# Kernel optimization log

Measured on AMD Instinct MI355X. Metric: run time of the kernel, lower is better.

The kernel has to match this reference:

```python
import jax, jax.numpy as jnp
import numpy as np

B, N, DM, H, C, DC = 4, 1024, 512, 8, 3, 16  # batch, nodes, node_dim, heads, manifold components, per-component dim
DK = DM // H


def setup_inputs() -> dict:
    key = jax.random.key(0)
    ks = jax.random.split(key, 8)

    def lin_w(k):
        return jax.random.normal(k, (DM, DM), jnp.float32) / np.sqrt(DM).astype(np.float32)

    return {
        "h": jax.random.normal(ks[0], (B, N, DM), jnp.float32),
        "x": jax.random.normal(ks[1], (B, N, C * DC), jnp.float32),
        "Wq": lin_w(ks[2]), "bq": jnp.zeros((DM,), jnp.float32),
        "Wk": lin_w(ks[3]), "bk": jnp.zeros((DM,), jnp.float32),
        "Wv": lin_w(ks[4]), "bv": jnp.zeros((DM,), jnp.float32),
        "Wo": lin_w(ks[5]), "bo": jnp.zeros((DM,), jnp.float32),
        "alpha": jnp.ones((H, C), jnp.float32),
        "log_sigma": jnp.zeros((H, C), jnp.float32),
    }


def reference(h, x, Wq, bq, Wk, bk, Wv, bv, Wo, bo, alpha, log_sigma):
    b, n, dm = h.shape
    hh, cc = alpha.shape
    dk = dm // hh
    scale = 1.0 / np.sqrt(dk).astype(np.float32)

    def to_heads(t, W, bias):
        return (t @ W.T + bias).reshape(b, n, hh, dk).transpose(0, 2, 1, 3)  # (B,H,N,dk)

    Q = to_heads(h, Wq, bq)
    K = to_heads(h, Wk, bk)
    V = to_heads(h, Wv, bv)

    attn = jnp.einsum('bhid,bhjd->bhij', Q, K) * scale  # (B,H,N,N)

    # Geodesic kernel: per-component Euclidean distances on the product manifold.
    xs = x.reshape(b, n, cc, -1)                      # (B,N,C,dc)
    sq = jnp.sum(xs * xs, axis=-1)                    # (B,N,C)
    inner = jnp.einsum('bicd,bjcd->bijc', xs, xs)     # (B,N,N,C)
    d_sq = jnp.maximum(sq[:, :, None, :] + sq[:, None, :, :] - 2.0 * inner, 0.0)  # (B,N,N,C)

    sigma = jnp.clip(jnp.exp(log_sigma), 1e-4)        # (H,C)
    # exp(-d_c^2 / (2 sigma_{h,c}^2)) -> (B,H,N,N,C), then weight by alpha and sum over c
    e = jnp.exp(-d_sq[:, None] / (2.0 * (sigma ** 2)[None, :, None, None, :])).astype(attn.dtype)
    attn = attn + jnp.einsum('hc,bhijc->bhij', alpha, e)

    p = jax.nn.softmax(attn, axis=-1)
    out = jnp.einsum('bhij,bhjd->bhid', p, V)         # (B,H,N,dk)
    out = out.transpose(0, 2, 1, 3).reshape(b, n, dm)
    return out @ Wo.T + bo
```

## Files before the change

kernel.cpp:

```cpp
#include <hip/hip_runtime.h>

typedef __bf16 bf16;
typedef __attribute__((ext_vector_type(8))) __bf16 bf16x8;
typedef __attribute__((ext_vector_type(4))) float f32x4;

#define LOG2E 1.44269504088896f
#define SCALE 0.125f

__device__ inline f32x4 mfma16(bf16x8 a, bf16x8 b, f32x4 c) {
    return __builtin_amdgcn_mfma_f32_16x16x32_bf16(a, b, c, 0, 0, 0);
}

__global__ __launch_bounds__(256) void prep_kernel(
        const float* __restrict__ h, const float* __restrict__ x,
        const float* __restrict__ Wq, const float* __restrict__ Wk,
        const float* __restrict__ Wv, const float* __restrict__ Wo,
        const float* __restrict__ bq, const float* __restrict__ bk,
        const float* __restrict__ bv,
        bf16* __restrict__ hb, bf16* __restrict__ wpack, bf16* __restrict__ wob,
        float* __restrict__ bqkv, bf16* __restrict__ xb, float* __restrict__ sqx) {
    int stride = gridDim.x * blockDim.x;
    int tid = blockIdx.x * blockDim.x + threadIdx.x;
    for (int i = tid; i < 4096 * 512; i += stride) hb[i] = (bf16)h[i];
    for (int i = tid; i < 3 * 512 * 512; i += stride) {
        float v = (i < 262144) ? Wq[i] : (i < 524288 ? Wk[i - 262144] : Wv[i - 524288]);
        wpack[i] = (bf16)v;
    }
    for (int i = tid; i < 512 * 512; i += stride) wob[i] = (bf16)Wo[i];
    for (int i = tid; i < 1536; i += stride)
        bqkv[i] = (i < 512) ? bq[i] : (i < 1024 ? bk[i - 512] : bv[i - 1024]);
    for (int i = tid; i < 4096 * 48; i += stride) xb[i] = (bf16)x[i];
    for (int i = tid; i < 4096 * 3; i += stride) {
        int row = i / 3, c = i - row * 3;
        float s = 0.0f;
        for (int k = 0; k < 16; k++) {
            float v = (float)(bf16)x[row * 48 + c * 16 + k];
            s += v * v;
        }
        sqx[i] = s;
    }
}

__global__ __launch_bounds__(256) void gemm_qkv_kernel(
        const bf16* __restrict__ A, const bf16* __restrict__ Bm,
        const float* __restrict__ bias,
        bf16* __restrict__ Qb, bf16* __restrict__ Kb, bf16* __restrict__ Vb) {
    __shared__ bf16 Al[64][72];
    __shared__ bf16 Bl[64][72];
    int t = threadIdx.x;
    int w = t >> 6, lane = t & 63, g = lane >> 4, lo = lane & 15;
    int rowbase = blockIdx.x * 64, colbase = blockIdx.y * 64;
    int wr = (w >> 1) * 32, wc = (w & 1) * 32;
    f32x4 acc[2][2] = {};
    int sr = t >> 2, sc = (t & 3) * 16;
    for (int kb = 0; kb < 512; kb += 64) {
        *(bf16x8*)&Al[sr][sc]     = *(const bf16x8*)&A[(rowbase + sr) * 512 + kb + sc];
        *(bf16x8*)&Al[sr][sc + 8] = *(const bf16x8*)&A[(rowbase + sr) * 512 + kb + sc + 8];
        *(bf16x8*)&Bl[sr][sc]     = *(const bf16x8*)&Bm[(colbase + sr) * 512 + kb + sc];
        *(bf16x8*)&Bl[sr][sc + 8] = *(const bf16x8*)&Bm[(colbase + sr) * 512 + kb + sc + 8];
        __syncthreads();
        for (int kk = 0; kk < 64; kk += 32) {
            bf16x8 af[2], bfr[2];
            af[0]  = *(const bf16x8*)&Al[wr + lo][kk + 8 * g];
            af[1]  = *(const bf16x8*)&Al[wr + 16 + lo][kk + 8 * g];
            bfr[0] = *(const bf16x8*)&Bl[wc + lo][kk + 8 * g];
            bfr[1] = *(const bf16x8*)&Bl[wc + 16 + lo][kk + 8 * g];
            for (int ri = 0; ri < 2; ri++)
                for (int ci = 0; ci < 2; ci++)
                    acc[ri][ci] = mfma16(af[ri], bfr[ci], acc[ri][ci]);
        }
        __syncthreads();
    }
    for (int ri = 0; ri < 2; ri++)
        for (int ci = 0; ci < 2; ci++) {
            int mcol = colbase + wc + 16 * ci + lo;
            float bv = bias[mcol];
            int proj = mcol >> 9, hm = mcol & 511, head = hm >> 6, d = hm & 63;
            bf16* dst = (proj == 0) ? Qb : (proj == 1 ? Kb : Vb);
            for (int r = 0; r < 4; r++) {
                int n = rowbase + wr + 16 * ri + 4 * g + r;
                int bidx = n >> 10, i = n & 1023;
                dst[((bidx * 8 + head) * 1024 + i) * 64 + d] = (bf16)(acc[ri][ci][r] + bv);
            }
        }
}

__global__ __launch_bounds__(256) void attn_kernel(
        const bf16* __restrict__ Qb, const bf16* __restrict__ Kb,
        const bf16* __restrict__ Vb, const bf16* __restrict__ xb,
        const float* __restrict__ sqx, const float* __restrict__ alpha,
        const float* __restrict__ log_sigma, bf16* __restrict__ attnout) {
    __shared__ bf16 Klds[64][72];
    __shared__ bf16 Xlds[64][56];
    __shared__ bf16 VTlds[64][72];
    __shared__ float sqj[3][64];
    __shared__ bf16 Plds[4][16][72];

    int t = threadIdx.x;
    int w = t >> 6, lane = t & 63, g = lane >> 4, lo = lane & 15;
    int b = blockIdx.z, hh = blockIdx.y;
    int i0 = blockIdx.x * 64 + w * 16;

    float alf[3], coef[3];
    for (int c = 0; c < 3; c++) {
        alf[c] = alpha[hh * 3 + c];
        float sg = expf(log_sigma[hh * 3 + c]);
        sg = fmaxf(sg, 1e-4f);
        coef[c] = -LOG2E / (2.0f * sg * sg);
    }

    const bf16* Qbase = Qb + ((size_t)(b * 8 + hh) * 1024 + i0) * 64;
    bf16x8 qa[2];
    qa[0] = *(const bf16x8*)&Qbase[lo * 64 + 8 * g];
    qa[1] = *(const bf16x8*)&Qbase[lo * 64 + 32 + 8 * g];

    bf16x8 xqa[3];
    const bf16* Xibase = xb + ((size_t)(b << 10) + i0) * 48;
    for (int c = 0; c < 3; c++) {
        bf16x8 v = {};
        if (g < 2) v = *(const bf16x8*)&Xibase[lo * 48 + c * 16 + 8 * g];
        xqa[c] = v;
    }

    float sqi[3][4];
    const float* sqibase = sqx + ((size_t)(b << 10) + i0) * 3;
    for (int r = 0; r < 4; r++)
        for (int c = 0; c < 3; c++) sqi[c][r] = sqibase[(4 * g + r) * 3 + c];

    float m_r[4], l_r[4];
    f32x4 o[4];
    for (int r = 0; r < 4; r++) { m_r[r] = -1e30f; l_r[r] = 0.0f; }
    for (int td = 0; td < 4; td++) o[td] = (f32x4){0.f, 0.f, 0.f, 0.f};

    int sr = t >> 2, sc = (t & 3) * 16;
    for (int j0 = 0; j0 < 1024; j0 += 64) {
        __syncthreads();
        const bf16* Kbase = Kb + ((size_t)(b * 8 + hh) * 1024 + j0) * 64;
        *(bf16x8*)&Klds[sr][sc]     = *(const bf16x8*)&Kbase[sr * 64 + sc];
        *(bf16x8*)&Klds[sr][sc + 8] = *(const bf16x8*)&Kbase[sr * 64 + sc + 8];
        const bf16* Vbase = Vb + ((size_t)(b * 8 + hh) * 1024 + j0) * 64;
        bf16x8 v0 = *(const bf16x8*)&Vbase[sr * 64 + sc];
        bf16x8 v1 = *(const bf16x8*)&Vbase[sr * 64 + sc + 8];
        for (int q = 0; q < 8; q++) VTlds[sc + q][sr] = v0[q];
        for (int q = 0; q < 8; q++) VTlds[sc + 8 + q][sr] = v1[q];
        for (int idx = t; idx < 384; idx += 256) {
            int xr = idx / 6, xc = (idx - xr * 6) * 8;
            *(bf16x8*)&Xlds[xr][xc] = *(const bf16x8*)&xb[((size_t)(b << 10) + j0 + xr) * 48 + xc];
        }
        if (t < 192) {
            int jl = t / 3, c = t - jl * 3;
            sqj[c][jl] = sqx[((size_t)(b << 10) + j0 + jl) * 3 + c];
        }
        __syncthreads();

        f32x4 s[4];
        for (int tt = 0; tt < 4; tt++) {
            f32x4 acc = {};
            bf16x8 kb0 = *(const bf16x8*)&Klds[16 * tt + lo][8 * g];
            bf16x8 kb1 = *(const bf16x8*)&Klds[16 * tt + lo][32 + 8 * g];
            acc = mfma16(qa[0], kb0, acc);
            acc = mfma16(qa[1], kb1, acc);
            f32x4 ic[3];
            for (int c = 0; c < 3; c++) {
                bf16x8 xbf = {};
                if (g < 2) xbf = *(const bf16x8*)&Xlds[16 * tt + lo][c * 16 + 8 * g];
                f32x4 z = {};
                ic[c] = mfma16(xqa[c], xbf, z);
            }
            for (int r = 0; r < 4; r++) {
                float sv = acc[r] * SCALE;
                for (int c = 0; c < 3; c++) {
                    float d = sqi[c][r] + sqj[c][16 * tt + lo] - 2.0f * ic[c][r];
                    d = fmaxf(d, 0.0f);
                    sv += alf[c] * exp2f(coef[c] * d);
                }
                acc[r] = sv;
            }
            s[tt] = acc;
        }

        float pm[4], sf[4], rs[4];
        for (int r = 0; r < 4; r++)
            pm[r] = fmaxf(fmaxf(s[0][r], s[1][r]), fmaxf(s[2][r], s[3][r]));
        for (int msk = 1; msk < 16; msk <<= 1)
            for (int r = 0; r < 4; r++) pm[r] = fmaxf(pm[r], __shfl_xor(pm[r], msk));
        for (int r = 0; r < 4; r++) {
            float mn = fmaxf(m_r[r], pm[r]);
            sf[r] = exp2f((m_r[r] - mn) * LOG2E);
            m_r[r] = mn;
            rs[r] = 0.0f;
        }
        for (int tt = 0; tt < 4; tt++)
            for (int r = 0; r < 4; r++) {
                float p = exp2f((s[tt][r] - m_r[r]) * LOG2E);
                s[tt][r] = p;
                rs[r] += p;
            }
        for (int msk = 1; msk < 16; msk <<= 1)
            for (int r = 0; r < 4; r++) rs[r] += __shfl_xor(rs[r], msk);
        for (int r = 0; r < 4; r++) l_r[r] = l_r[r] * sf[r] + rs[r];

        for (int tt = 0; tt < 4; tt++)
            for (int r = 0; r < 4; r++)
                Plds[w][4 * g + r][16 * tt + lo] = (bf16)s[tt][r];

        for (int td = 0; td < 4; td++)
            for (int r = 0; r < 4; r++) o[td][r] *= sf[r];

        bf16x8 pa0 = *(const bf16x8*)&Plds[w][lo][8 * g];
        bf16x8 pa1 = *(const bf16x8*)&Plds[w][lo][32 + 8 * g];
        for (int td = 0; td < 4; td++) {
            bf16x8 vb0 = *(const bf16x8*)&VTlds[16 * td + lo][8 * g];
            bf16x8 vb1 = *(const bf16x8*)&VTlds[16 * td + lo][32 + 8 * g];
            o[td] = mfma16(pa0, vb0, o[td]);
            o[td] = mfma16(pa1, vb1, o[td]);
        }
    }

    for (int td = 0; td < 4; td++)
        for (int r = 0; r < 4; r++) {
            float val = o[td][r] / l_r[r];
            int i = i0 + 4 * g + r;
            attnout[((size_t)(b << 10) + i) * 512 + hh * 64 + 16 * td + lo] = (bf16)val;
        }
}

__global__ __launch_bounds__(256) void gemm_out_kernel(
        const bf16* __restrict__ A, const bf16* __restrict__ Bm,
        const float* __restrict__ bias, float* __restrict__ out) {
    __shared__ bf16 Al[64][72];
    __shared__ bf16 Bl[64][72];
    int t = threadIdx.x;
    int w = t >> 6, lane = t & 63, g = lane >> 4, lo = lane & 15;
    int rowbase = blockIdx.x * 64, colbase = blockIdx.y * 64;
    int wr = (w >> 1) * 32, wc = (w & 1) * 32;
    f32x4 acc[2][2] = {};
    int sr = t >> 2, sc = (t & 3) * 16;
    for (int kb = 0; kb < 512; kb += 64) {
        *(bf16x8*)&Al[sr][sc]     = *(const bf16x8*)&A[(rowbase + sr) * 512 + kb + sc];
        *(bf16x8*)&Al[sr][sc + 8] = *(const bf16x8*)&A[(rowbase + sr) * 512 + kb + sc + 8];
        *(bf16x8*)&Bl[sr][sc]     = *(const bf16x8*)&Bm[(colbase + sr) * 512 + kb + sc];
        *(bf16x8*)&Bl[sr][sc + 8] = *(const bf16x8*)&Bm[(colbase + sr) * 512 + kb + sc + 8];
        __syncthreads();
        for (int kk = 0; kk < 64; kk += 32) {
            bf16x8 af[2], bfr[2];
            af[0]  = *(const bf16x8*)&Al[wr + lo][kk + 8 * g];
            af[1]  = *(const bf16x8*)&Al[wr + 16 + lo][kk + 8 * g];
            bfr[0] = *(const bf16x8*)&Bl[wc + lo][kk + 8 * g];
            bfr[1] = *(const bf16x8*)&Bl[wc + 16 + lo][kk + 8 * g];
            for (int ri = 0; ri < 2; ri++)
                for (int ci = 0; ci < 2; ci++)
                    acc[ri][ci] = mfma16(af[ri], bfr[ci], acc[ri][ci]);
        }
        __syncthreads();
    }
    for (int ri = 0; ri < 2; ri++)
        for (int ci = 0; ci < 2; ci++) {
            int mcol = colbase + wc + 16 * ci + lo;
            float bv = bias[mcol];
            for (int r = 0; r < 4; r++) {
                int n = rowbase + wr + 16 * ri + 4 * g + r;
                out[(size_t)n * 512 + mcol] = acc[ri][ci][r] + bv;
            }
        }
}

extern "C" void kernel_launch(void* const* d_in, const int* in_sizes, int n_in,
                              void* d_out, int out_size, void* d_ws, size_t ws_size,
                              hipStream_t stream) {
    const float* h  = (const float*)d_in[0];
    const float* x  = (const float*)d_in[1];
    const float* Wq = (const float*)d_in[2];
    const float* bq = (const float*)d_in[3];
    const float* Wk = (const float*)d_in[4];
    const float* bk = (const float*)d_in[5];
    const float* Wv = (const float*)d_in[6];
    const float* bv = (const float*)d_in[7];
    const float* Wo = (const float*)d_in[8];
    const float* bo = (const float*)d_in[9];
    const float* alpha     = (const float*)d_in[10];
    const float* log_sigma = (const float*)d_in[11];
    float* out = (float*)d_out;

    char* ws = (char*)d_ws;
    size_t off = 0;
    auto alloc = [&](size_t bytes) {
        char* p = ws + off;
        off += (bytes + 255) & ~(size_t)255;
        return p;
    };
    bf16*  hb      = (bf16*)alloc(4096 * 512 * 2);
    bf16*  wpack   = (bf16*)alloc(1536 * 512 * 2);
    bf16*  wob     = (bf16*)alloc(512 * 512 * 2);
    float* bqkv    = (float*)alloc(1536 * 4);
    bf16*  xb      = (bf16*)alloc(4096 * 48 * 2);
    float* sqx     = (float*)alloc(4096 * 3 * 4);
    bf16*  Qb      = (bf16*)alloc((size_t)4 * 8 * 1024 * 64 * 2);
    bf16*  Kb      = (bf16*)alloc((size_t)4 * 8 * 1024 * 64 * 2);
    bf16*  Vb      = (bf16*)alloc((size_t)4 * 8 * 1024 * 64 * 2);
    bf16*  attnout = (bf16*)alloc(4096 * 512 * 2);

    prep_kernel<<<512, 256, 0, stream>>>(h, x, Wq, Wk, Wv, Wo, bq, bk, bv,
                                         hb, wpack, wob, bqkv, xb, sqx);
    gemm_qkv_kernel<<<dim3(64, 24), 256, 0, stream>>>(hb, wpack, bqkv, Qb, Kb, Vb);
    attn_kernel<<<dim3(16, 8, 4), 256, 0, stream>>>(Qb, Kb, Vb, xb, sqx,
                                                    alpha, log_sigma, attnout);
    gemm_out_kernel<<<dim3(64, 8), 256, 0, stream>>>(attnout, wob, bo, out);
}
```

Baseline: 202.6 us.

## Split attention over key range and store V pre-transposed

The attention kernel now splits the key dimension into up to two halves across extra blocks and writes unnormalised partial outputs plus running max and sum to workspace. A new merge kernel combines them with log-sum-exp weights. The QKV GEMM also writes V transposed so the attention kernel can load it with vector copies instead of scalar LDS transposes. The aim is to raise occupancy, since the original grid has only 512 blocks, and to cut the LDS transpose cost. The price is one extra launch and float partial-result traffic through global memory.

New measurement: 211.0 us. 4.2% more time.

```diff
diff --git a/kernel.cpp b/kernel.cpp
--- a/kernel.cpp
+++ b/kernel.cpp
@@ -44,7 +44,7 @@
 __global__ __launch_bounds__(256) void gemm_qkv_kernel(
         const bf16* __restrict__ A, const bf16* __restrict__ Bm,
         const float* __restrict__ bias,
-        bf16* __restrict__ Qb, bf16* __restrict__ Kb, bf16* __restrict__ Vb) {
+        bf16* __restrict__ Qb, bf16* __restrict__ Kb, bf16* __restrict__ Vt) {
     __shared__ bf16 Al[64][72];
     __shared__ bf16 Bl[64][72];
     int t = threadIdx.x;
@@ -76,20 +76,26 @@
             int mcol = colbase + wc + 16 * ci + lo;
             float bv = bias[mcol];
             int proj = mcol >> 9, hm = mcol & 511, head = hm >> 6, d = hm & 63;
-            bf16* dst = (proj == 0) ? Qb : (proj == 1 ? Kb : Vb);
             for (int r = 0; r < 4; r++) {
                 int n = rowbase + wr + 16 * ri + 4 * g + r;
                 int bidx = n >> 10, i = n & 1023;
-                dst[((bidx * 8 + head) * 1024 + i) * 64 + d] = (bf16)(acc[ri][ci][r] + bv);
+                bf16 val = (bf16)(acc[ri][ci][r] + bv);
+                if (proj == 0)
+                    Qb[((size_t)(bidx * 8 + head) * 1024 + i) * 64 + d] = val;
+                else if (proj == 1)
+                    Kb[((size_t)(bidx * 8 + head) * 1024 + i) * 64 + d] = val;
+                else
+                    Vt[((size_t)(bidx * 8 + head) * 64 + d) * 1024 + i] = val;
             }
         }
 }
 
 __global__ __launch_bounds__(256) void attn_kernel(
         const bf16* __restrict__ Qb, const bf16* __restrict__ Kb,
-        const bf16* __restrict__ Vb, const bf16* __restrict__ xb,
+        const bf16* __restrict__ Vt, const bf16* __restrict__ xb,
         const float* __restrict__ sqx, const float* __restrict__ alpha,
-        const float* __restrict__ log_sigma, bf16* __restrict__ attnout) {
+        const float* __restrict__ log_sigma, int nsplit,
+        float* __restrict__ o_part, float* __restrict__ ml_part) {
     __shared__ bf16 Klds[64][72];
     __shared__ bf16 Xlds[64][56];
     __shared__ bf16 VTlds[64][72];
@@ -98,7 +104,9 @@
 
     int t = threadIdx.x;
     int w = t >> 6, lane = t & 63, g = lane >> 4, lo = lane & 15;
-    int b = blockIdx.z, hh = blockIdx.y;
+    int zz = blockIdx.z;
+    int b = zz / nsplit, split = zz - b * nsplit;
+    int hh = blockIdx.y;
     int i0 = blockIdx.x * 64 + w * 16;
 
     float alf[3], coef[3];
@@ -133,16 +141,15 @@
     for (int td = 0; td < 4; td++) o[td] = (f32x4){0.f, 0.f, 0.f, 0.f};
 
     int sr = t >> 2, sc = (t & 3) * 16;
-    for (int j0 = 0; j0 < 1024; j0 += 64) {
+    int jlen = 1024 / nsplit, jb = split * jlen;
+    for (int j0 = jb; j0 < jb + jlen; j0 += 64) {
         __syncthreads();
         const bf16* Kbase = Kb + ((size_t)(b * 8 + hh) * 1024 + j0) * 64;
         *(bf16x8*)&Klds[sr][sc]     = *(const bf16x8*)&Kbase[sr * 64 + sc];
         *(bf16x8*)&Klds[sr][sc + 8] = *(const bf16x8*)&Kbase[sr * 64 + sc + 8];
-        const bf16* Vbase = Vb + ((size_t)(b * 8 + hh) * 1024 + j0) * 64;
-        bf16x8 v0 = *(const bf16x8*)&Vbase[sr * 64 + sc];
-        bf16x8 v1 = *(const bf16x8*)&Vbase[sr * 64 + sc + 8];
-        for (int q = 0; q < 8; q++) VTlds[sc + q][sr] = v0[q];
-        for (int q = 0; q < 8; q++) VTlds[sc + 8 + q][sr] = v1[q];
+        const bf16* Vbase = Vt + ((size_t)(b * 8 + hh) * 64) * 1024 + j0;
+        *(bf16x8*)&VTlds[sr][sc]     = *(const bf16x8*)&Vbase[sr * 1024 + sc];
+        *(bf16x8*)&VTlds[sr][sc + 8] = *(const bf16x8*)&Vbase[sr * 1024 + sc + 8];
         for (int idx = t; idx < 384; idx += 256) {
             int xr = idx / 6, xc = (idx - xr * 6) * 8;
             *(bf16x8*)&Xlds[xr][xc] = *(const bf16x8*)&xb[((size_t)(b << 10) + j0 + xr) * 48 + xc];
@@ -219,10 +226,42 @@
 
     for (int td = 0; td < 4; td++)
         for (int r = 0; r < 4; r++) {
-            float val = o[td][r] / l_r[r];
             int i = i0 + 4 * g + r;
-            attnout[((size_t)(b << 10) + i) * 512 + hh * 64 + 16 * td + lo] = (bf16)val;
-        }
+            size_t rowg = (size_t)(b * 8 + hh) * 1024 + i;
+            o_part[((size_t)split * 32768 + rowg) * 64 + 16 * td + lo] = o[td][r];
+        }
+    if (lo == 0)
+        for (int r = 0; r < 4; r++) {
+            int i = i0 + 4 * g + r;
+            size_t rowg = (size_t)(b * 8 + hh) * 1024 + i;
+            ml_part[((size_t)split * 32768 + rowg) * 2]     = m_r[r];
+            ml_part[((size_t)split * 32768 + rowg) * 2 + 1] = l_r[r];
+        }
+}
+
+__global__ __launch_bounds__(256) void merge_kernel(
+        const float* __restrict__ o_part, const float* __restrict__ ml_part,
+        int nsplit, bf16* __restrict__ attnout) {
+    int t = threadIdx.x;
+    int rowg = blockIdx.x * 16 + (t >> 4);
+    int d4 = (t & 15) * 4;
+    float m0 = ml_part[(size_t)rowg * 2], l0 = ml_part[(size_t)rowg * 2 + 1];
+    float m1 = -1e30f, l1 = 0.0f;
+    if (nsplit == 2) {
+        m1 = ml_part[((size_t)32768 + rowg) * 2];
+        l1 = ml_part[((size_t)32768 + rowg) * 2 + 1];
+    }
+    float M = fmaxf(m0, m1);
+    float w0 = exp2f((m0 - M) * LOG2E);
+    float w1 = exp2f((m1 - M) * LOG2E);
+    float inv = 1.0f / (w0 * l0 + w1 * l1);
+    f32x4 a = *(const f32x4*)&o_part[(size_t)rowg * 64 + d4];
+    f32x4 bv = (f32x4){0.f, 0.f, 0.f, 0.f};
+    if (nsplit == 2) bv = *(const f32x4*)&o_part[((size_t)32768 + rowg) * 64 + d4];
+    int b = rowg >> 13, hh = (rowg >> 10) & 7, i = rowg & 1023;
+    bf16* dst = &attnout[((size_t)(b << 10) + i) * 512 + hh * 64 + d4];
+    for (int q = 0; q < 4; q++)
+        dst[q] = (bf16)((w0 * a[q] + w1 * bv[q]) * inv);
 }
 
 __global__ __launch_bounds__(256) void gemm_out_kernel(
@@ -297,13 +336,20 @@
     float* sqx     = (float*)alloc(4096 * 3 * 4);
     bf16*  Qb      = (bf16*)alloc((size_t)4 * 8 * 1024 * 64 * 2);
     bf16*  Kb      = (bf16*)alloc((size_t)4 * 8 * 1024 * 64 * 2);
-    bf16*  Vb      = (bf16*)alloc((size_t)4 * 8 * 1024 * 64 * 2);
+    bf16*  Vt      = (bf16*)alloc((size_t)4 * 8 * 1024 * 64 * 2);
     bf16*  attnout = (bf16*)alloc(4096 * 512 * 2);
+    size_t base = off;
+
+    size_t need2 = base + 2 * ((size_t)32768 * 64 * 4 + 1024) + 2 * ((size_t)32768 * 2 * 4 + 1024);
+    int nsplit = (ws_size >= need2) ? 2 : 1;
+    float* o_part  = (float*)alloc((size_t)nsplit * 32768 * 64 * 4);
+    float* ml_part = (float*)alloc((size_t)nsplit * 32768 * 2 * 4);
 
     prep_kernel<<<512, 256, 0, stream>>>(h, x, Wq, Wk, Wv, Wo, bq, bk, bv,
                                          hb, wpack, wob, bqkv, xb, sqx);
-    gemm_qkv_kernel<<<dim3(64, 24), 256, 0, stream>>>(hb, wpack, bqkv, Qb, Kb, Vb);
-    attn_kernel<<<dim3(16, 8, 4), 256, 0, stream>>>(Qb, Kb, Vb, xb, sqx,
-                                                    alpha, log_sigma, attnout);
+    gemm_qkv_kernel<<<dim3(64, 24), 256, 0, stream>>>(hb, wpack, bqkv, Qb, Kb, Vt);
+    attn_kernel<<<dim3(16, 8, 4 * nsplit), 256, 0, stream>>>(
+        Qb, Kb, Vt, xb, sqx, alpha, log_sigma, nsplit, o_part, ml_part);
+    merge_kernel<<<2048, 256, 0, stream>>>(o_part, ml_part, nsplit, attnout);
     gemm_out_kernel<<<dim3(64, 8), 256, 0, stream>>>(attnout, wob, bo, out);
 }
```
